# Kernel optimization log

Hardware: AMD Instinct MI355X
Metric: run time of the kernel (lower is better)

## Reference

```python
import jax, jax.numpy as jnp
import numpy as np

G = 8            # n_group
C = 256          # input_dim / channels
N_MEM = C // G   # 32
ALPHA = 0.4      # w_alpha
EPS = 1e-5
SLOPE = 0.01     # LeakyReLU negative slope


def _lrelu(x):
    return jnp.where(x >= 0, x, SLOPE * x)


def _mlp(x, ws, bs):
    # torch nn.Linear convention: y = x @ W.T + b; lrelu on all but last layer
    n = len(ws)
    for i in range(n):
        x = x @ ws[i].T + bs[i]
        if i < n - 1:
            x = _lrelu(x)
    return x


def _wct(c_A, s_B, mask, ct_ws, ct_bs, mu_ws, mu_bs):
    B, Cc, H, W = c_A.shape
    n_mem = Cc // G
    # style -> per-group coloring matrices  (Get.coloring, vectorized over groups)
    s_CT = _mlp(s_B.reshape(B * G, n_mem), ct_ws, ct_bs).reshape(B, G, n_mem, n_mem)
    D = jnp.sqrt(jnp.sum(s_CT ** 2, axis=2, keepdims=True))        # [B,G,1,n_mem]
    U = s_CT / D                                                    # column-normalized
    UDU = jnp.einsum('bgij,bgkj->bgik', s_CT, U)                    # [B,G,n_mem,n_mem]
    # torch.cat(U_arr, dim=0) is group-major: index g*B+b
    eigen_s = jnp.transpose(U, (1, 0, 2, 3)).reshape(G * B, n_mem, n_mem)
    X = jnp.tile(UDU.reshape(B, Cc, n_mem), (1, 1, G)) * mask       # [B,C,C]
    s_mu = _mlp(s_B, mu_ws, mu_bs)[:, :, None, None]                # [B,C,1,1]
    # per-group covariance of mean-centered content
    c_g = jnp.transpose(c_A, (1, 0, 2, 3)).reshape(G, n_mem, B * H * W)
    c_g = c_g - jnp.mean(c_g, axis=2, keepdims=True)
    cov_c = jnp.einsum('gin,gjn->gij', c_g, c_g) / (B * H * W - 1) \
        + EPS * jnp.eye(n_mem, dtype=c_A.dtype)
    # centered content, reinterpreted as [B, C, H*W] (matches torch view/permute)
    whitend = jnp.transpose(c_g.reshape(Cc, B, H * W), (1, 0, 2))
    colored = jnp.einsum('bcd,bdn->bcn', X, whitend).reshape(B, Cc, H, W)
    out = ALPHA * (colored + s_mu) + (1.0 - ALPHA) * c_A
    return out, cov_c, eigen_s


def setup_inputs():
    key = jax.random.key(0)
    ks = jax.random.split(key, 16)
    B, H, W = 4, 128, 128
    c_A = jax.random.normal(ks[0], (B, C, H, W), dtype=jnp.float32)
    s_B = jax.random.normal(ks[1], (B, C), dtype=jnp.float32)
    # block-diagonal group mask [1, C, C]
    m = np.zeros((C, C), dtype=np.float32)
    for g in range(G):
        m[g * N_MEM:(g + 1) * N_MEM, g * N_MEM:(g + 1) * N_MEM] = 1.0
    mask = jnp.asarray(m)[None]

    def lin(k, o, i):
        return jax.random.normal(k, (o, i), dtype=jnp.float32) * (1.0 / np.sqrt(i))

    inp = {'c_A': c_A, 's_B': s_B, 'mask': mask}
    dims_ct = [(256, 32), (256, 256), (256, 256), (256, 256), (1024, 256)]
    for j, (o, i) in enumerate(dims_ct):
        inp['ct_w%d' % j] = lin(ks[2 + j], o, i)
        inp['ct_b%d' % j] = jnp.zeros((o,), dtype=jnp.float32)
    dims_mu = [(256, 256), (256, 256), (256, 256)]
    for j, (o, i) in enumerate(dims_mu):
        inp['mu_w%d' % j] = lin(ks[8 + j], o, i)
        inp['mu_b%d' % j] = jnp.zeros((o,), dtype=jnp.float32)
    return inp


def reference(c_A, s_B, mask, ct_w0, ct_b0, ct_w1, ct_b1, ct_w2, ct_b2,
              ct_w3, ct_b3, ct_w4, ct_b4, mu_w0, mu_b0, mu_w1, mu_b1,
              mu_w2, mu_b2):
    ct_ws = (ct_w0, ct_w1, ct_w2, ct_w3, ct_w4)
    ct_bs = (ct_b0, ct_b1, ct_b2, ct_b3, ct_b4)
    mu_ws = (mu_w0, mu_w1, mu_w2)
    mu_bs = (mu_b0, mu_b1, mu_b2)
    return _wct(c_A, s_B, mask, ct_ws, ct_bs, mu_ws, mu_bs)
```

## Files before the change

kernel.cpp:

```cpp
#include <hip/hip_runtime.h>
#include <hip/hip_bf16.h>

typedef __bf16 bf16x8 __attribute__((ext_vector_type(8)));
typedef float  f32x16 __attribute__((ext_vector_type(16)));

#define ALPHA_W 0.4f
#define NTOT 65536.0f

#define OUT_MAIN 16777216
#define OUT_COV  (OUT_MAIN)
#define OUT_EIG  (OUT_MAIN + 8192)

struct WP {
    const float* cw0; const float* cb0;
    const float* cw1; const float* cb1;
    const float* cw2; const float* cb2;
    const float* cw3; const float* cb3;
    const float* cw4; const float* cb4;
    const float* mw0; const float* mb0;
    const float* mw1; const float* mb1;
    const float* mw2; const float* mb2;
};

struct SJ { const float* X; const float* W; const float* B; float* Y; int ld; int act; };

__device__ __forceinline__ float lrelu(float x) { return x >= 0.f ? x : 0.01f * x; }

template<int ROWS, int IN, int KS, int NCB, int ACT>
__device__ __forceinline__ void lin_block(const float* __restrict__ X,
                                          const float* __restrict__ Wg,
                                          const float* __restrict__ Bs,
                                          float* __restrict__ Y, int ld,
                                          int bidl, int tid) {
    constexpr int SL = IN / KS;
    constexpr int SF4 = SL / 4;
    int s = tid % KS;
    int r = (tid / KS) % ROWS;
    int c = tid / (KS * ROWS);
    int col = bidl * NCB + c;
    const float4* wp = (const float4*)(Wg + (size_t)col * IN + s * SL);
    const float4* xp = (const float4*)(X + r * IN + s * SL);
    float a0 = 0.f, a1 = 0.f, a2 = 0.f, a3 = 0.f;
    #pragma unroll
    for (int i = 0; i < SF4; ++i) {
        float4 wv = wp[i];
        float4 xv = xp[i];
        a0 = fmaf(wv.x, xv.x, a0); a1 = fmaf(wv.y, xv.y, a1);
        a2 = fmaf(wv.z, xv.z, a2); a3 = fmaf(wv.w, xv.w, a3);
    }
    float v = (a0 + a1) + (a2 + a3);
    #pragma unroll
    for (int m = 1; m < KS; m <<= 1) v += __shfl_xor(v, m, 64);
    if (s == 0) {
        float o = v + Bs[col];
        if (ACT) o = lrelu(o);
        Y[(size_t)r * ld + col] = o;
    }
}

template<int SPG>
__global__ __launch_bounds__(256, 2) void front(const float* __restrict__ cA,
                                                const float* __restrict__ sB,
                                                WP wp,
                                                float* __restrict__ pSXY,
                                                float* __restrict__ pSX,
                                                float* __restrict__ XA,
                                                float* __restrict__ MUA) {
    int bid = blockIdx.x;
    int tid = threadIdx.x;
    if (bid < 64) {
        if (bid < 32) {
            lin_block<32, 32, 1, 8, 1>(sB, wp.cw0, wp.cb0, XA, 256, bid, tid);
        } else {
            lin_block<4, 256, 8, 8, 1>(sB, wp.mw0, wp.mb0, MUA, 256, bid - 32, tid);
        }
        return;
    }
    constexpr int PSZ = 65536 / SPG;
    constexpr int ITS = PSZ / 64;
    int gbid = bid - 64;
    int g = gbid / SPG, slice = gbid % SPG;
    int w = tid >> 6, l = tid & 63;
    int col = l & 31, kq = l >> 5;
    int nbase = slice * PSZ + w * (PSZ / 4);
    int b = nbase >> 14, hw0 = nbase & 16383;
    const float* base = cA + (((size_t)(b * 256 + g * 32 + col)) << 14) + hw0 + kq * 8;
    f32x16 acc;
    #pragma unroll
    for (int r = 0; r < 16; r++) acc[r] = 0.f;
    float s0 = 0.f, s1 = 0.f;
    #pragma unroll 8
    for (int it = 0; it < ITS; ++it) {
        float4 f0 = *(const float4*)(base + it * 16);
        float4 f1 = *(const float4*)(base + it * 16 + 4);
        s0 += (f0.x + f0.y) + (f0.z + f0.w);
        s1 += (f1.x + f1.y) + (f1.z + f1.w);
        bf16x8 v;
        v[0] = (__bf16)f0.x; v[1] = (__bf16)f0.y; v[2] = (__bf16)f0.z; v[3] = (__bf16)f0.w;
        v[4] = (__bf16)f1.x; v[5] = (__bf16)f1.y; v[6] = (__bf16)f1.z; v[7] = (__bf16)f1.w;
        acc = __builtin_amdgcn_mfma_f32_32x32x16_bf16(v, v, acc, 0, 0, 0);
    }
    __shared__ float red[4][1024];
    __shared__ float sxr[4][64];
    sxr[w][l] = s0 + s1;
    #pragma unroll
    for (int r = 0; r < 16; r++) {
        int i = (r & 3) + 8 * (r >> 2) + 4 * kq;
        red[w][i * 32 + col] = acc[r];
    }
    __syncthreads();
    for (int e = tid; e < 1024; e += 256)
        pSXY[(size_t)gbid * 1024 + e] = red[0][e] + red[1][e] + red[2][e] + red[3][e];
    if (tid < 32) {
        float v = 0.f;
        #pragma unroll
        for (int ww = 0; ww < 4; ww++) v += sxr[ww][tid] + sxr[ww][tid + 32];
        pSX[gbid * 32 + tid] = v;
    }
}

__global__ __launch_bounds__(256) void stage(SJ a, SJ m, int nbA) {
    int bid = blockIdx.x, tid = threadIdx.x;
    if (bid < nbA) {
        if (a.act) lin_block<32, 256, 4, 2, 1>(a.X, a.W, a.B, a.Y, a.ld, bid, tid);
        else       lin_block<32, 256, 4, 2, 0>(a.X, a.W, a.B, a.Y, a.ld, bid, tid);
    } else {
        int bl = bid - nbA;
        if (m.act) lin_block<4, 256, 8, 8, 1>(m.X, m.W, m.B, m.Y, m.ld, bl, tid);
        else       lin_block<4, 256, 8, 8, 0>(m.X, m.W, m.B, m.Y, m.ld, bl, tid);
    }
}

template<int SPG>
__global__ __launch_bounds__(256, 2) void finalize(const float* __restrict__ CT,
                                                   const float* __restrict__ SMU,
                                                   const float* __restrict__ pSXY,
                                                   const float* __restrict__ pSX,
                                                   float* __restrict__ M,
                                                   float* __restrict__ T,
                                                   float* __restrict__ out) {
    int bid = blockIdx.x, t = threadIdx.x;
    __shared__ float sxg[32];
    if (bid < 32) {
        int b = bid >> 3, g = bid & 7;
        __shared__ float sct[32 * 33], uu[32 * 33], ud[32 * 33], dinv[32];
        for (int e = t; e < 1024; e += 256) sct[(e >> 5) * 33 + (e & 31)] = CT[bid * 1024 + e];
        if (t < 32) {
            float s = 0.f;
            #pragma unroll 8
            for (int sl = 0; sl < SPG; sl++) s += pSX[(g * SPG + sl) * 32 + t];
            sxg[t] = s * (1.0f / NTOT);
        }
        __syncthreads();
        if (t < 32) {
            float s = 0.f;
            #pragma unroll
            for (int i = 0; i < 32; i++) { float v = sct[i * 33 + t]; s = fmaf(v, v, s); }
            dinv[t] = 1.0f / sqrtf(s);
        }
        __syncthreads();
        float* eig = out + OUT_EIG + (size_t)(g * 4 + b) * 1024;
        for (int e = t; e < 1024; e += 256) {
            int i = e >> 5, jj = e & 31;
            float u = sct[i * 33 + jj] * dinv[jj];
            uu[i * 33 + jj] = u;
            eig[e] = u;
        }
        __syncthreads();
        float* Mo = M + (size_t)bid * 1024;
        for (int e = t; e < 1024; e += 256) {
            int i = e >> 5, k = e & 31;
            float s = 0.f;
            #pragma unroll
            for (int jv = 0; jv < 32; jv++) s = fmaf(sct[i * 33 + jv], uu[k * 33 + jv], s);
            ud[i * 33 + k] = s;
            Mo[e] = ALPHA_W * s + (i == k ? (1.0f - ALPHA_W) : 0.0f);
        }
        __syncthreads();
        if (t < 32) {
            float s = 0.f;
            #pragma unroll
            for (int k = 0; k < 32; k++) s = fmaf(ud[t * 33 + k], sxg[k], s);
            T[bid * 32 + t] = ALPHA_W * (SMU[bid * 32 + t] - s);
        }
    } else {
        int g = bid - 32;
        if (t < 32) {
            float s = 0.f;
            #pragma unroll 8
            for (int sl = 0; sl < SPG; sl++) s += pSX[(g * SPG + sl) * 32 + t];
            sxg[t] = s * (1.0f / NTOT);
        }
        __syncthreads();
        float* cov = out + OUT_COV + (size_t)g * 1024;
        for (int e = t; e < 1024; e += 256) {
            float s = 0.f;
            #pragma unroll 8
            for (int sl = 0; sl < SPG; sl++) s += pSXY[(size_t)(g * SPG + sl) * 1024 + e];
            int i = e >> 5, jj = e & 31;
            float vv = (s - NTOT * sxg[i] * sxg[jj]) * (1.0f / (NTOT - 1.0f));
            if (i == jj) vv += 1e-5f;
            cov[e] = vv;
        }
    }
}

__global__ __launch_bounds__(256) void color_k(const float* __restrict__ cA,
                                               const float* __restrict__ M,
                                               const float* __restrict__ T,
                                               float* __restrict__ out) {
    __shared__ float Ml[1024];
    __shared__ float tl[32];
    int bid = blockIdx.x;
    int tid = threadIdx.x;
    int bg = bid >> 5, chunk = bid & 31;
    int b = bg >> 3, g = bg & 7;

    for (int e = tid; e < 1024; e += 256) Ml[e] = M[(size_t)bg * 1024 + e];
    if (tid < 32) tl[tid] = T[bg * 32 + tid];
    __syncthreads();

    int ci = tid >> 6;
    int pj = tid & 63;
    size_t rowbase = ((size_t)(b * 256 + g * 32)) << 14;
    int px = chunk * 512 + pj * 8;
    const float* xsrc = cA + rowbase + px;
    float* dst = out + rowbase + (((size_t)ci * 8) << 14) + px;

    float acc[8][8];
    #pragma unroll
    for (int c = 0; c < 8; ++c) {
        float t0 = tl[ci * 8 + c];
        #pragma unroll
        for (int j = 0; j < 8; ++j) acc[c][j] = t0;
    }
    #pragma unroll 4
    for (int k = 0; k < 32; ++k) {
        const float* xk = xsrc + ((size_t)k << 14);
        float4 x0 = *(const float4*)xk;
        float4 x1 = *(const float4*)(xk + 4);
        #pragma unroll
        for (int c = 0; c < 8; ++c) {
            float m = Ml[(ci * 8 + c) * 32 + k];
            acc[c][0] = fmaf(m, x0.x, acc[c][0]);
            acc[c][1] = fmaf(m, x0.y, acc[c][1]);
            acc[c][2] = fmaf(m, x0.z, acc[c][2]);
            acc[c][3] = fmaf(m, x0.w, acc[c][3]);
            acc[c][4] = fmaf(m, x1.x, acc[c][4]);
            acc[c][5] = fmaf(m, x1.y, acc[c][5]);
            acc[c][6] = fmaf(m, x1.z, acc[c][6]);
            acc[c][7] = fmaf(m, x1.w, acc[c][7]);
        }
    }
    #pragma unroll
    for (int c = 0; c < 8; ++c) {
        float4 o0 = {acc[c][0], acc[c][1], acc[c][2], acc[c][3]};
        float4 o1 = {acc[c][4], acc[c][5], acc[c][6], acc[c][7]};
        float* d = dst + (((size_t)c) << 14);
        *(float4*)d = o0;
        *(float4*)(d + 4) = o1;
    }
}

extern "C" void kernel_launch(void* const* d_in, const int* in_sizes, int n_in,
                              void* d_out, int out_size, void* d_ws, size_t ws_size,
                              hipStream_t stream) {
    (void)in_sizes; (void)n_in; (void)out_size;
    const float* cA = (const float*)d_in[0];
    const float* sB = (const float*)d_in[1];
    WP wp;
    wp.cw0 = (const float*)d_in[3];  wp.cb0 = (const float*)d_in[4];
    wp.cw1 = (const float*)d_in[5];  wp.cb1 = (const float*)d_in[6];
    wp.cw2 = (const float*)d_in[7];  wp.cb2 = (const float*)d_in[8];
    wp.cw3 = (const float*)d_in[9];  wp.cb3 = (const float*)d_in[10];
    wp.cw4 = (const float*)d_in[11]; wp.cb4 = (const float*)d_in[12];
    wp.mw0 = (const float*)d_in[13]; wp.mb0 = (const float*)d_in[14];
    wp.mw1 = (const float*)d_in[15]; wp.mb1 = (const float*)d_in[16];
    wp.mw2 = (const float*)d_in[17]; wp.mb2 = (const float*)d_in[18];
    float* W = (float*)d_ws;
    float* out = (float*)d_out;

    bool big = ws_size >= (size_t)6 * 1024 * 1024;
    int NSL = big ? 1024 : 512;
    size_t oPSX = (size_t)NSL * 1024;
    size_t base = oPSX + (size_t)NSL * 32;
    float* pSXY = W;
    float* pSX  = W + oPSX;
    float* XA   = W + base;
    float* XB   = XA + 8192;
    float* MUA  = XB + 8192;
    float* MUB  = MUA + 1024;
    float* SMU  = MUB + 1024;
    float* CT   = SMU + 1024;
    float* Mw   = CT + 32768;
    float* Tw   = Mw + 32768;

    if (big) front<128><<<64 + 1024, 256, 0, stream>>>(cA, sB, wp, pSXY, pSX, XA, MUA);
    else     front<64><<<64 + 512, 256, 0, stream>>>(cA, sB, wp, pSXY, pSX, XA, MUA);

    SJ a, m;
    a = {XA, wp.cw1, wp.cb1, XB, 256, 1};
    m = {MUA, wp.mw1, wp.mb1, MUB, 256, 1};
    stage<<<160, 256, 0, stream>>>(a, m, 128);
    a = {XB, wp.cw2, wp.cb2, XA, 256, 1};
    m = {MUB, wp.mw2, wp.mb2, SMU, 256, 0};
    stage<<<160, 256, 0, stream>>>(a, m, 128);
    a = {XA, wp.cw3, wp.cb3, XB, 256, 1};
    stage<<<128, 256, 0, stream>>>(a, a, 128);
    a = {XB, wp.cw4, wp.cb4, CT, 1024, 0};
    stage<<<512, 256, 0, stream>>>(a, a, 512);

    if (big) finalize<128><<<40, 256, 0, stream>>>(CT, SMU, pSXY, pSX, Mw, Tw, out);
    else     finalize<64><<<40, 256, 0, stream>>>(CT, SMU, pSXY, pSX, Mw, Tw, out);

    color_k<<<1024, 256, 0, stream>>>(cA, Mw, Tw, out);
}
```

Measured before the change: 232.4 us.

## Stage color tile through LDS and fix front split to 64 slices per group

The coloring kernel now copies each 32-channel by 256-pixel tile of content into shared memory in two halves, using coalesced float4 loads. Each thread then computes 8 channels by 4 strided pixels from LDS and writes scalar, coalesced outputs. Before, each thread streamed strided float4 rows straight from global memory. The front/finalize kernels drop the workspace-size-dependent template choice and always use 64 slices per group with fixed workspace offsets. The trade-offs are 32KB of LDS per block, added barriers, and less parallelism in the covariance pass when the workspace is large.

```diff
diff --git a/kernel.cpp b/kernel.cpp
--- a/kernel.cpp
+++ b/kernel.cpp
@@ -10,6 +10,17 @@
 #define OUT_MAIN 16777216
 #define OUT_COV  (OUT_MAIN)
 #define OUT_EIG  (OUT_MAIN + 8192)
+
+#define WS_PSXY  0
+#define WS_PSX   524288
+#define WS_XA    540672
+#define WS_XB    548864
+#define WS_MUA   557056
+#define WS_MUB   558080
+#define WS_SMU   559104
+#define WS_CT    560128
+#define WS_M     592896
+#define WS_T     625664
 
 struct WP {
     const float* cw0; const float* cb0;
@@ -58,7 +69,6 @@
     }
 }
 
-template<int SPG>
 __global__ __launch_bounds__(256, 2) void front(const float* __restrict__ cA,
                                                 const float* __restrict__ sB,
                                                 WP wp,
@@ -76,13 +86,11 @@
         }
         return;
     }
-    constexpr int PSZ = 65536 / SPG;
-    constexpr int ITS = PSZ / 64;
     int gbid = bid - 64;
-    int g = gbid / SPG, slice = gbid % SPG;
+    int g = gbid >> 6, slice = gbid & 63;
     int w = tid >> 6, l = tid & 63;
     int col = l & 31, kq = l >> 5;
-    int nbase = slice * PSZ + w * (PSZ / 4);
+    int nbase = slice * 1024 + w * 256;
     int b = nbase >> 14, hw0 = nbase & 16383;
     const float* base = cA + (((size_t)(b * 256 + g * 32 + col)) << 14) + hw0 + kq * 8;
     f32x16 acc;
@@ -90,7 +98,7 @@
     for (int r = 0; r < 16; r++) acc[r] = 0.f;
     float s0 = 0.f, s1 = 0.f;
     #pragma unroll 8
-    for (int it = 0; it < ITS; ++it) {
+    for (int it = 0; it < 16; ++it) {
         float4 f0 = *(const float4*)(base + it * 16);
         float4 f1 = *(const float4*)(base + it * 16 + 4);
         s0 += (f0.x + f0.y) + (f0.z + f0.w);
@@ -131,7 +139,6 @@
     }
 }
 
-template<int SPG>
 __global__ __launch_bounds__(256, 2) void finalize(const float* __restrict__ CT,
                                                    const float* __restrict__ SMU,
                                                    const float* __restrict__ pSXY,
@@ -148,7 +155,7 @@
         if (t < 32) {
             float s = 0.f;
             #pragma unroll 8
-            for (int sl = 0; sl < SPG; sl++) s += pSX[(g * SPG + sl) * 32 + t];
+            for (int sl = 0; sl < 64; sl++) s += pSX[(g * 64 + sl) * 32 + t];
             sxg[t] = s * (1.0f / NTOT);
         }
         __syncthreads();
@@ -188,7 +195,7 @@
         if (t < 32) {
             float s = 0.f;
             #pragma unroll 8
-            for (int sl = 0; sl < SPG; sl++) s += pSX[(g * SPG + sl) * 32 + t];
+            for (int sl = 0; sl < 64; sl++) s += pSX[(g * 64 + sl) * 32 + t];
             sxg[t] = s * (1.0f / NTOT);
         }
         __syncthreads();
@@ -196,7 +203,7 @@
         for (int e = t; e < 1024; e += 256) {
             float s = 0.f;
             #pragma unroll 8
-            for (int sl = 0; sl < SPG; sl++) s += pSXY[(size_t)(g * SPG + sl) * 1024 + e];
+            for (int sl = 0; sl < 64; sl++) s += pSXY[(size_t)(g * 64 + sl) * 1024 + e];
             int i = e >> 5, jj = e & 31;
             float vv = (s - NTOT * sxg[i] * sxg[jj]) * (1.0f / (NTOT - 1.0f));
             if (i == jj) vv += 1e-5f;
@@ -205,10 +212,11 @@
     }
 }
 
-__global__ __launch_bounds__(256) void color_k(const float* __restrict__ cA,
-                                               const float* __restrict__ M,
-                                               const float* __restrict__ T,
-                                               float* __restrict__ out) {
+__global__ __launch_bounds__(256, 2) void color_k(const float* __restrict__ cA,
+                                                  const float* __restrict__ M,
+                                                  const float* __restrict__ T,
+                                                  float* __restrict__ out) {
+    __shared__ float xs[32 * 256];
     __shared__ float Ml[1024];
     __shared__ float tl[32];
     int bid = blockIdx.x;
@@ -218,54 +226,54 @@
 
     for (int e = tid; e < 1024; e += 256) Ml[e] = M[(size_t)bg * 1024 + e];
     if (tid < 32) tl[tid] = T[bg * 32 + tid];
-    __syncthreads();
-
-    int ci = tid >> 6;
-    int pj = tid & 63;
+
     size_t rowbase = ((size_t)(b * 256 + g * 32)) << 14;
-    int px = chunk * 512 + pj * 8;
-    const float* xsrc = cA + rowbase + px;
-    float* dst = out + rowbase + (((size_t)ci * 8) << 14) + px;
-
-    float acc[8][8];
-    #pragma unroll
-    for (int c = 0; c < 8; ++c) {
-        float t0 = tl[ci * 8 + c];
+    int ih = tid >> 6, n = tid & 63;
+    int sch = tid >> 3, sp = (tid & 7) * 4;
+
+    for (int half = 0; half < 2; ++half) {
+        const float* src = cA + rowbase + ((size_t)sch << 14) + chunk * 512 + half * 256 + sp;
+        float* dstl = xs + sch * 256 + sp;
         #pragma unroll
-        for (int j = 0; j < 8; ++j) acc[c][j] = t0;
-    }
-    #pragma unroll 4
-    for (int k = 0; k < 32; ++k) {
-        const float* xk = xsrc + ((size_t)k << 14);
-        float4 x0 = *(const float4*)xk;
-        float4 x1 = *(const float4*)(xk + 4);
+        for (int i = 0; i < 8; ++i)
+            *(float4*)(dstl + i * 32) = *(const float4*)(src + i * 32);
+        __syncthreads();
+
+        float acc[8][4];
         #pragma unroll
         for (int c = 0; c < 8; ++c) {
-            float m = Ml[(ci * 8 + c) * 32 + k];
-            acc[c][0] = fmaf(m, x0.x, acc[c][0]);
-            acc[c][1] = fmaf(m, x0.y, acc[c][1]);
-            acc[c][2] = fmaf(m, x0.z, acc[c][2]);
-            acc[c][3] = fmaf(m, x0.w, acc[c][3]);
-            acc[c][4] = fmaf(m, x1.x, acc[c][4]);
-            acc[c][5] = fmaf(m, x1.y, acc[c][5]);
-            acc[c][6] = fmaf(m, x1.z, acc[c][6]);
-            acc[c][7] = fmaf(m, x1.w, acc[c][7]);
-        }
-    }
-    #pragma unroll
-    for (int c = 0; c < 8; ++c) {
-        float4 o0 = {acc[c][0], acc[c][1], acc[c][2], acc[c][3]};
-        float4 o1 = {acc[c][4], acc[c][5], acc[c][6], acc[c][7]};
-        float* d = dst + (((size_t)c) << 14);
-        *(float4*)d = o0;
-        *(float4*)(d + 4) = o1;
+            float t0 = tl[ih * 8 + c];
+            #pragma unroll
+            for (int t = 0; t < 4; ++t) acc[c][t] = t0;
+        }
+        #pragma unroll 4
+        for (int k = 0; k < 32; ++k) {
+            float m[8];
+            #pragma unroll
+            for (int c = 0; c < 8; ++c) m[c] = Ml[(ih * 8 + c) * 32 + k];
+            float xv[4];
+            #pragma unroll
+            for (int t = 0; t < 4; ++t) xv[t] = xs[k * 256 + t * 64 + n];
+            #pragma unroll
+            for (int c = 0; c < 8; ++c)
+                #pragma unroll
+                for (int t = 0; t < 4; ++t)
+                    acc[c][t] = fmaf(m[c], xv[t], acc[c][t]);
+        }
+        #pragma unroll
+        for (int c = 0; c < 8; ++c) {
+            float* d = out + rowbase + (((size_t)(ih * 8 + c)) << 14) + chunk * 512 + half * 256 + n;
+            #pragma unroll
+            for (int t = 0; t < 4; ++t) d[t * 64] = acc[c][t];
+        }
+        __syncthreads();
     }
 }
 
 extern "C" void kernel_launch(void* const* d_in, const int* in_sizes, int n_in,
                               void* d_out, int out_size, void* d_ws, size_t ws_size,
                               hipStream_t stream) {
-    (void)in_sizes; (void)n_in; (void)out_size;
+    (void)in_sizes; (void)n_in; (void)out_size; (void)ws_size;
     const float* cA = (const float*)d_in[0];
     const float* sB = (const float*)d_in[1];
     WP wp;
@@ -280,38 +288,21 @@
     float* W = (float*)d_ws;
     float* out = (float*)d_out;
 
-    bool big = ws_size >= (size_t)6 * 1024 * 1024;
-    int NSL = big ? 1024 : 512;
-    size_t oPSX = (size_t)NSL * 1024;
-    size_t base = oPSX + (size_t)NSL * 32;
-    float* pSXY = W;
-    float* pSX  = W + oPSX;
-    float* XA   = W + base;
-    float* XB   = XA + 8192;
-    float* MUA  = XB + 8192;
-    float* MUB  = MUA + 1024;
-    float* SMU  = MUB + 1024;
-    float* CT   = SMU + 1024;
-    float* Mw   = CT + 32768;
-    float* Tw   = Mw + 32768;
-
-    if (big) front<128><<<64 + 1024, 256, 0, stream>>>(cA, sB, wp, pSXY, pSX, XA, MUA);
-    else     front<64><<<64 + 512, 256, 0, stream>>>(cA, sB, wp, pSXY, pSX, XA, MUA);
-
+    front<<<576, 256, 0, stream>>>(cA, sB, wp, W + WS_PSXY, W + WS_PSX,
+                                   W + WS_XA, W + WS_MUA);
     SJ a, m;
-    a = {XA, wp.cw1, wp.cb1, XB, 256, 1};
-    m = {MUA, wp.mw1, wp.mb1, MUB, 256, 1};
+    a = {W + WS_XA, wp.cw1, wp.cb1, W + WS_XB, 256, 1};
+    m = {W + WS_MUA, wp.mw1, wp.mb1, W + WS_MUB, 256, 1};
     stage<<<160, 256, 0, stream>>>(a, m, 128);
-    a = {XB, wp.cw2, wp.cb2, XA, 256, 1};
-    m = {MUB, wp.mw2, wp.mb2, SMU, 256, 0};
+    a = {W + WS_XB, wp.cw2, wp.cb2, W + WS_XA, 256, 1};
+    m = {W + WS_MUB, wp.mw2, wp.mb2, W + WS_SMU, 256, 0};
     stage<<<160, 256, 0, stream>>>(a, m, 128);
-    a = {XA, wp.cw3, wp.cb3, XB, 256, 1};
+    a = {W + WS_XA, wp.cw3, wp.cb3, W + WS_XB, 256, 1};
     stage<<<128, 256, 0, stream>>>(a, a, 128);
-    a = {XB, wp.cw4, wp.cb4, CT, 1024, 0};
+    a = {W + WS_XB, wp.cw4, wp.cb4, W + WS_CT, 1024, 0};
     stage<<<512, 256, 0, stream>>>(a, a, 512);
 
-    if (big) finalize<128><<<40, 256, 0, stream>>>(CT, SMU, pSXY, pSX, Mw, Tw, out);
-    else     finalize<64><<<40, 256, 0, stream>>>(CT, SMU, pSXY, pSX, Mw, Tw, out);
-
-    color_k<<<1024, 256, 0, stream>>>(cA, Mw, Tw, out);
-}
+    finalize<<<40, 256, 0, stream>>>(W + WS_CT, W + WS_SMU, W + WS_PSXY, W + WS_PSX,
+                                     W + WS_M, W + WS_T, out);
+    color_k<<<1024, 256, 0, stream>>>(cA, W + WS_M, W + WS_T, out);
+}
```

Measured after the change: 205.4 us. 1.13x faster.
